# Kernel tuning notes

Measured on AMD Instinct MI355X. Metric: run time of the kernel, lower is better.

The kernel has to match this reference:

```python
import jax, jax.numpy as jnp
import numpy as np

B, S, D = 2, 1024, 4096
NQ, NKV, HD = 32, 8, 128
G = NQ // NKV
FFN = 10928  # ffn_size(4096, 4.0): int(4*4096)*2//3 = 10922 -> round up to mult of 8
ATTN_MULT = 0.08838834764831845
MAX_ATTN = 30.0
EPS = 1e-5
BASE = 10000.0


def setup_inputs() -> dict:
    key = jax.random.key(0)
    ks = jax.random.split(key, 13)
    def w(k, shape):
        return jax.random.normal(k, shape, jnp.float32) / np.float32(np.sqrt(shape[0]))
    return {
        "x": jax.random.normal(ks[0], (B, S, D), jnp.float32),
        "mask": jnp.tril(jnp.ones((1, 1, S, S), dtype=bool)),  # causal
        "scale_pre_attn": jax.random.uniform(ks[1], (D,), jnp.float32, 0.5, 1.5),
        "scale_post_attn": jax.random.uniform(ks[2], (D,), jnp.float32, 0.5, 1.5),
        "scale_pre_mlp": jax.random.uniform(ks[3], (D,), jnp.float32, 0.5, 1.5),
        "scale_post_mlp": jax.random.uniform(ks[4], (D,), jnp.float32, 0.5, 1.5),
        "wq": w(ks[5], (D, NQ * HD)),
        "wk": w(ks[6], (D, NKV * HD)),
        "wv": w(ks[7], (D, NKV * HD)),
        "wo": w(ks[8], (NQ * HD, D)),
        "w_gate": w(ks[9], (D, FFN)),
        "w_val": w(ks[10], (D, FFN)),
        "w_out": w(ks[11], (FFN, D)),
    }


def rms_norm(x, scale):
    ms = jnp.mean(jnp.square(x), axis=-1, keepdims=True)
    return x * jax.lax.rsqrt(ms + EPS) * scale


def rotate_half(x):
    x1, x2 = jnp.split(x, 2, axis=-1)
    return jnp.concatenate((-x2, x1), axis=-1)


def apply_rope(x):
    # x: [b, s, h, d]; offset=0 (no KV-cache step)
    s, d = x.shape[1], x.shape[3]
    inv_freq = 1.0 / (BASE ** (jnp.arange(0, d, 2, dtype=jnp.float32) / d))
    t = jnp.arange(s, dtype=jnp.float32)
    phase = t[:, None] * inv_freq[None, :]            # [s, d/2]
    phase = jnp.tile(phase, (1, 2))[None, :, None, :]  # [1, s, 1, d]
    return (x * jnp.cos(phase) + rotate_half(x) * jnp.sin(phase)).astype(x.dtype)


def reference(x, mask, scale_pre_attn, scale_post_attn, scale_pre_mlp, scale_post_mlp,
              wq, wk, wv, wo, w_gate, w_val, w_out):
    h = x
    # ---- attention sublayer (pre-norm) ----
    hn = rms_norm(h, scale_pre_attn)
    q = (hn @ wq).reshape(B, S, NQ, HD)
    k = (hn @ wk).reshape(B, S, NKV, HD)
    v = (hn @ wv).reshape(B, S, NKV, HD)
    q = apply_rope(q)
    k = apply_rope(k)
    qg = q.reshape(B, S, NKV, G, HD)  # GQA: group q heads per kv head
    logits = jnp.einsum("btkgd,bskd->bkgts", qg, k).astype(jnp.float32) * ATTN_MULT
    logits = MAX_ATTN * jnp.tanh(logits / MAX_ATTN)   # grok soft cap
    logits = jnp.where(mask[:, :, None], logits, -1e30)
    probs = jax.nn.softmax(logits, axis=-1).astype(x.dtype)
    attn = jnp.einsum("bkgts,bskd->btkgd", probs, v).reshape(B, S, NQ * HD)
    h_attn = attn @ wo
    h = h + rms_norm(h_attn, scale_post_attn)
    # ---- gated MLP sublayer (pre-norm) ----
    hn2 = rms_norm(h, scale_pre_mlp)
    h_dense = (jax.nn.gelu(hn2 @ w_gate) * (hn2 @ w_val)) @ w_out
    h = h + rms_norm(h_dense, scale_post_mlp)
    return h
```

## Files before the change

### kernel.cpp

```cpp
#include <hip/hip_runtime.h>
#include <stdint.h>

typedef unsigned short ushort_t;
typedef unsigned short us8 __attribute__((ext_vector_type(8)));
typedef __bf16 bf16x8 __attribute__((ext_vector_type(8)));
typedef float f32x4 __attribute__((ext_vector_type(4)));

#define D_MODEL 4096
#define SEQ 1024
#define BROWS 2048
#define QKV_N 6144
#define HD 128
#define FFN_GRID 11008
#define ATTN_MULT 0.08838834764831845f

__device__ __forceinline__ unsigned short f2bf(float f){
  union { float f; unsigned u; } c; c.f = f;
  unsigned u = c.u + 0x7fffu + ((c.u >> 16) & 1u);
  return (unsigned short)(u >> 16);
}
__device__ __forceinline__ float bf2f(unsigned short h){
  union { unsigned u; float f; } c; c.u = ((unsigned)h) << 16;
  return c.f;
}
__device__ __forceinline__ f32x4 zero4(){ f32x4 z; z[0]=0.f; z[1]=0.f; z[2]=0.f; z[3]=0.f; return z; }
__device__ __forceinline__ bf16x8 ldb8(const void* p){ return *(const bf16x8*)p; }
__device__ __forceinline__ f32x4 MFMA(bf16x8 a, bf16x8 b, f32x4 c){
  return __builtin_amdgcn_mfma_f32_16x16x32_bf16(a, b, c, 0, 0, 0);
}
__device__ __forceinline__ void g2lds16(void* lds, const void* g){
  __builtin_amdgcn_global_load_lds(
      (const __attribute__((address_space(1))) void*)(uintptr_t)(g),
      (__attribute__((address_space(3))) void*)(uint32_t)(uintptr_t)(lds),
      16, 0, 0);
}
#define BAR() __builtin_amdgcn_s_barrier()
#define VMCNT8() asm volatile("s_waitcnt vmcnt(8)" ::: "memory")
#define VMCNT0() asm volatile("s_waitcnt vmcnt(0)" ::: "memory")
#define SGB0() __builtin_amdgcn_sched_barrier(0)

__global__ __launch_bounds__(256) void rmsnorm_in(const float* __restrict__ x,
                                                  const float* __restrict__ sc,
                                                  ushort_t* __restrict__ out){
  int row = blockIdx.x, tid = threadIdx.x;
  const float4* xr = (const float4*)(x + (size_t)row*D_MODEL);
  float4 v[4]; float ss = 0.f;
#pragma unroll
  for (int i=0;i<4;i++){
    v[i] = xr[tid + i*256];
    ss += v[i].x*v[i].x + v[i].y*v[i].y + v[i].z*v[i].z + v[i].w*v[i].w;
  }
#pragma unroll
  for (int m=32;m;m>>=1) ss += __shfl_xor(ss, m);
  __shared__ float red[4];
  if ((tid&63)==0) red[tid>>6] = ss;
  __syncthreads();
  float inv = rsqrtf((red[0]+red[1]+red[2]+red[3])*(1.f/4096.f) + 1e-5f);
  const float4* scv = (const float4*)sc;
#pragma unroll
  for (int i=0;i<4;i++){
    float4 s4 = scv[tid + i*256];
    ushort4 o;
    o.x = f2bf(v[i].x*inv*s4.x); o.y = f2bf(v[i].y*inv*s4.y);
    o.z = f2bf(v[i].z*inv*s4.z); o.w = f2bf(v[i].w*inv*s4.w);
    ((ushort4*)out)[(size_t)row*1024 + tid + i*256] = o;
  }
}

__global__ __launch_bounds__(256) void rmsnorm_resid(const float* __restrict__ base,
                                                     const float* __restrict__ delta,
                                                     const float* __restrict__ delta2,
                                                     const float* __restrict__ sc1,
                                                     float* __restrict__ hout,
                                                     const float* __restrict__ sc2,
                                                     ushort_t* __restrict__ hn2){
  int row = blockIdx.x, tid = threadIdx.x;
  const float4* dr = (const float4*)(delta + (size_t)row*D_MODEL);
  const float4* d2 = delta2 ? (const float4*)(delta2 + (size_t)row*D_MODEL) : nullptr;
  const float4* br = (const float4*)(base  + (size_t)row*D_MODEL);
  float4 d[4]; float ss = 0.f;
#pragma unroll
  for (int i=0;i<4;i++){
    float4 a = dr[tid + i*256];
    if (d2){
      float4 b = d2[tid + i*256];
      a.x += b.x; a.y += b.y; a.z += b.z; a.w += b.w;
    }
    d[i] = a;
    ss += d[i].x*d[i].x + d[i].y*d[i].y + d[i].z*d[i].z + d[i].w*d[i].w;
  }
#pragma unroll
  for (int m=32;m;m>>=1) ss += __shfl_xor(ss, m);
  __shared__ float red[4];
  if ((tid&63)==0) red[tid>>6] = ss;
  __syncthreads();
  float inv1 = rsqrtf((red[0]+red[1]+red[2]+red[3])*(1.f/4096.f) + 1e-5f);
  const float4* s1v = (const float4*)sc1;
  float4* ho = (float4*)(hout + (size_t)row*D_MODEL);
  float4 h4[4]; float ss2 = 0.f;
#pragma unroll
  for (int i=0;i<4;i++){
    float4 b4 = br[tid + i*256];
    float4 s4 = s1v[tid + i*256];
    float4 h;
    h.x = b4.x + d[i].x*inv1*s4.x;
    h.y = b4.y + d[i].y*inv1*s4.y;
    h.z = b4.z + d[i].z*inv1*s4.z;
    h.w = b4.w + d[i].w*inv1*s4.w;
    h4[i] = h;
    ho[tid + i*256] = h;
    ss2 += h.x*h.x + h.y*h.y + h.z*h.z + h.w*h.w;
  }
  if (sc2){
#pragma unroll
    for (int m=32;m;m>>=1) ss2 += __shfl_xor(ss2, m);
    __syncthreads();
    if ((tid&63)==0) red[tid>>6] = ss2;
    __syncthreads();
    float inv2 = rsqrtf((red[0]+red[1]+red[2]+red[3])*(1.f/4096.f) + 1e-5f);
    const float4* s2v = (const float4*)sc2;
#pragma unroll
    for (int i=0;i<4;i++){
      float4 s4 = s2v[tid + i*256];
      ushort4 o;
      o.x = f2bf(h4[i].x*inv2*s4.x); o.y = f2bf(h4[i].y*inv2*s4.y);
      o.z = f2bf(h4[i].z*inv2*s4.z); o.w = f2bf(h4[i].w*inv2*s4.w);
      ((ushort4*)hn2)[(size_t)row*1024 + tid + i*256] = o;
    }
  }
}

__global__ __launch_bounds__(256) void convT(const float* __restrict__ W,
                                             ushort_t* __restrict__ WT,
                                             int K, int N, int Kp, int Np){
  __shared__ float tile[64][69];
  int tx = threadIdx.x & 15, ty = threadIdx.x >> 4;
  int n0 = blockIdx.x*64, k0 = blockIdx.y*64;
#pragma unroll
  for (int i=0;i<4;i++){
    int k = k0 + ty + i*16, n = n0 + tx*4;
    float4 v;
    if (k < K && n + 3 < N){
      v = *(const float4*)&W[(size_t)k*N + n];
    } else {
      v.x = (k<K && n+0<N) ? W[(size_t)k*N + n+0] : 0.f;
      v.y = (k<K && n+1<N) ? W[(size_t)k*N + n+1] : 0.f;
      v.z = (k<K && n+2<N) ? W[(size_t)k*N + n+2] : 0.f;
      v.w = (k<K && n+3<N) ? W[(size_t)k*N + n+3] : 0.f;
    }
    tile[ty+i*16][tx*4+0] = v.x;
    tile[ty+i*16][tx*4+1] = v.y;
    tile[ty+i*16][tx*4+2] = v.z;
    tile[ty+i*16][tx*4+3] = v.w;
  }
  __syncthreads();
  int kc = (threadIdx.x & 7)*8, nr = threadIdx.x >> 3;
#pragma unroll
  for (int j=0;j<2;j++){
    int n = n0 + nr + j*32;
    if (n < Np){
      us8 o;
#pragma unroll
      for (int i=0;i<8;i++) o[i] = f2bf(tile[kc+i][nr + j*32]);
      *(us8*)&WT[(size_t)n*Kp + k0 + kc] = o;
    }
  }
}

template<int MODE, int KS>
__global__ __launch_bounds__(512, 2) void gemmW(const ushort_t* __restrict__ A, int lda,
                                                const ushort_t* __restrict__ WT, int ldw,
                                                void* __restrict__ Cv, void* __restrict__ Cv2,
                                                int ldc, int Nvalid, int K){
  __shared__ __align__(16) char smem[131072];
  const int nwg = gridDim.x;
  const int lid = blockIdx.x;
  int t = (lid & 7) * (nwg >> 3) + (lid >> 3);
  void* Cout = Cv;
  if (KS == 2){
    const int per = nwg >> 1;
    if (t >= per){ t -= per; A += (size_t)K; WT += (size_t)K; Cout = Cv2; }
  }
  const int m0 = (t & 7) << 8;
  const int n0 = (t >> 3) << 8;
  const int tid = threadIdx.x;
  const int w = tid >> 6, lane = tid & 63;
  const int wm = w >> 1, wn = w & 1;
  const int lo = lane & 15, hi = lane >> 4;
  const int srow = lane >> 3, scol = lane & 7;
  const int sw = scol ^ srow;
  const int rsw = lo & 7;
  const int NT = K >> 6;

  const ushort_t* pA = A  + (size_t)(m0 + w*8 + srow) * lda + sw*8;
  const ushort_t* pB = WT + (size_t)(n0 + w*8 + srow) * ldw + sw*8;

  auto stage = [&](int tt, int c){
    const ushort_t* g = (c < 4 ? pA + (size_t)(c*64)*lda : pB + (size_t)((c-4)*64)*ldw) + (size_t)tt*64;
    g2lds16(smem + ((tt&1)<<16) + (c < 4 ? c*8192 : 32768 + (c-4)*8192) + (w<<10), g);
  };

  f32x4 acc[4][8];
#pragma unroll
  for (int i=0;i<4;i++)
#pragma unroll
    for (int j=0;j<8;j++) acc[i][j] = zero4();

#pragma unroll
  for (int c=0;c<8;c++) stage(0, c);
#pragma unroll
  for (int c=0;c<8;c++) stage(1, c);

  for (int i=0;i<NT;i++){
    if (i == NT-1) VMCNT0(); else VMCNT8();
    BAR();
    const char* sA = smem + ((i&1)<<16);
    const char* sB = sA + 32768;
    bf16x8 af[4][2], bfr[8][2];
#pragma unroll
    for (int rf=0;rf<4;rf++)
#pragma unroll
      for (int kc=0;kc<2;kc++)
        af[rf][kc] = ldb8(sA + (wm*64 + rf*16 + lo)*128 + (((kc*4+hi)^rsw)<<4));
#pragma unroll
    for (int cf=0;cf<8;cf++)
#pragma unroll
      for (int kc=0;kc<2;kc++)
        bfr[cf][kc] = ldb8(sB + (wn*128 + cf*16 + lo)*128 + (((kc*4+hi)^rsw)<<4));
#pragma unroll
    for (int rf=0;rf<4;rf++)
#pragma unroll
      for (int cf=0;cf<8;cf++)
#pragma unroll
        for (int kc=0;kc<2;kc++)
          acc[rf][cf] = MFMA(af[rf][kc], bfr[cf][kc], acc[rf][cf]);
    SGB0();
    BAR();
    if (i+2 < NT){
#pragma unroll
      for (int c=0;c<8;c++) stage(i+2, c);
    }
  }
#pragma unroll
  for (int rf=0;rf<4;rf++){
#pragma unroll
    for (int cf=0;cf<8;cf++){
#pragma unroll
      for (int r=0;r<4;r++){
        int m = m0 + wm*64 + rf*16 + hi*4 + r;
        int n = n0 + wn*128 + cf*16 + lo;
        if (n < Nvalid){
          float v = acc[rf][cf][r];
          size_t idx = (size_t)m*ldc + n;
          if (MODE == 1) ((float*)Cout)[idx] = v;
          else           ((ushort_t*)Cout)[idx] = f2bf(v);
        }
      }
    }
  }
}

__global__ __launch_bounds__(512, 2) void gemm_gv(const ushort_t* __restrict__ A, int lda,
                                                  const ushort_t* __restrict__ B1,
                                                  const ushort_t* __restrict__ B2, int ldw,
                                                  ushort_t* __restrict__ Cv, int ldc,
                                                  int Nvalid, int K){
  __shared__ __align__(16) char smem[131072];
  const int nwg = gridDim.x;
  const int lid = blockIdx.x;
  const int t  = (lid & 7) * (nwg >> 3) + (lid >> 3);
  const int m0 = (t & 7) << 8;
  const int n0 = (t >> 3) << 7;
  const int tid = threadIdx.x;
  const int w = tid >> 6, lane = tid & 63;
  const int wm = w >> 1, wn = w & 1;
  const int lo = lane & 15, hi = lane >> 4;
  const int srow = lane >> 3, scol = lane & 7;
  const int sw = scol ^ srow;
  const int rsw = lo & 7;
  const int NT = K >> 6;

  const ushort_t* pA  = A  + (size_t)(m0 + w*8 + srow) * lda + sw*8;
  const ushort_t* pB1 = B1 + (size_t)(n0 + w*8 + srow) * ldw + sw*8;
  const ushort_t* pB2 = B2 + (size_t)(n0 + w*8 + srow) * ldw + sw*8;

  auto stage = [&](int tt, int c){
    const ushort_t* g;
    int lofs;
    if (c < 4){ g = pA  + (size_t)(c*64)*lda;     lofs = c*8192; }
    else if (c < 6){ g = pB1 + (size_t)((c-4)*64)*ldw; lofs = 32768 + (c-4)*8192; }
    else { g = pB2 + (size_t)((c-6)*64)*ldw; lofs = 49152 + (c-6)*8192; }
    g2lds16(smem + ((tt&1)<<16) + lofs + (w<<10), g + (size_t)tt*64);
  };

  f32x4 ag[4][4], av[4][4];
#pragma unroll
  for (int i=0;i<4;i++)
#pragma unroll
    for (int j=0;j<4;j++){ ag[i][j] = zero4(); av[i][j] = zero4(); }

#pragma unroll
  for (int c=0;c<8;c++) stage(0, c);
#pragma unroll
  for (int c=0;c<8;c++) stage(1, c);

  for (int i=0;i<NT;i++){
    if (i == NT-1) VMCNT0(); else VMCNT8();
    BAR();
    const char* sA  = smem + ((i&1)<<16);
    const char* sB1 = sA + 32768;
    const char* sB2 = sA + 49152;
    bf16x8 af[4][2], b1f[4][2], b2f[4][2];
#pragma unroll
    for (int rf=0;rf<4;rf++)
#pragma unroll
      for (int kc=0;kc<2;kc++)
        af[rf][kc] = ldb8(sA + (wm*64 + rf*16 + lo)*128 + (((kc*4+hi)^rsw)<<4));
#pragma unroll
    for (int cf=0;cf<4;cf++)
#pragma unroll
      for (int kc=0;kc<2;kc++){
        b1f[cf][kc] = ldb8(sB1 + (wn*64 + cf*16 + lo)*128 + (((kc*4+hi)^rsw)<<4));
        b2f[cf][kc] = ldb8(sB2 + (wn*64 + cf*16 + lo)*128 + (((kc*4+hi)^rsw)<<4));
      }
#pragma unroll
    for (int rf=0;rf<4;rf++)
#pragma unroll
      for (int cf=0;cf<4;cf++)
#pragma unroll
        for (int kc=0;kc<2;kc++){
          ag[rf][cf] = MFMA(af[rf][kc], b1f[cf][kc], ag[rf][cf]);
          av[rf][cf] = MFMA(af[rf][kc], b2f[cf][kc], av[rf][cf]);
        }
    SGB0();
    BAR();
    if (i+2 < NT){
#pragma unroll
      for (int c=0;c<8;c++) stage(i+2, c);
    }
  }
#pragma unroll
  for (int rf=0;rf<4;rf++){
#pragma unroll
    for (int cf=0;cf<4;cf++){
#pragma unroll
      for (int r=0;r<4;r++){
        int m = m0 + wm*64 + rf*16 + hi*4 + r;
        int n = n0 + wn*64 + cf*16 + lo;
        if (n < Nvalid){
          float g = ag[rf][cf][r];
          float v = av[rf][cf][r];
          float ga = 0.5f*g*(1.f + tanhf(0.7978845608028654f*(g + 0.044715f*g*g*g)));
          Cv[(size_t)m*ldc + n] = f2bf(ga * v);
        }
      }
    }
  }
}

__global__ void rope_tab_kernel(float* __restrict__ tab){
  int s = blockIdx.x, i = threadIdx.x;
  float invf = __expf(-(float)i * (9.210340371976184f/64.f));
  float ph = (float)s * invf;
  float sn, cs;
  sincosf(ph, &sn, &cs);
  tab[s*128 + i] = cs;
  tab[s*128 + 64 + i] = sn;
}

__global__ __launch_bounds__(256) void rope_apply(ushort_t* __restrict__ qkv,
                                                  const float* __restrict__ tab){
  int idx = blockIdx.x*256 + threadIdx.x;
  int pr = idx & 63;
  int h  = (idx >> 6) % 40;
  int row = idx / 2560;
  int t = row & (SEQ-1);
  ushort_t* p = qkv + (size_t)row*QKV_N + h*HD + pr;
  float c = tab[t*128 + pr], s = tab[t*128 + 64 + pr];
  float x1 = bf2f(p[0]), x2 = bf2f(p[64]);
  p[0]  = f2bf(x1*c - x2*s);
  p[64] = f2bf(x2*c + x1*s);
}

__global__ __launch_bounds__(256) void transpose_v(const ushort_t* __restrict__ qkv,
                                                   ushort_t* __restrict__ VT){
  __shared__ ushort_t tile[32][33];
  int d0 = blockIdx.x*32, m0 = blockIdx.y*32;
  int tx = threadIdx.x & 31, ty = threadIdx.x >> 5;
#pragma unroll
  for (int i=0;i<4;i++)
    tile[ty + i*8][tx] = qkv[(size_t)(m0 + ty + i*8)*QKV_N + 5120 + d0 + tx];
  __syncthreads();
#pragma unroll
  for (int i=0;i<4;i++)
    VT[(size_t)(d0 + ty + i*8)*BROWS + m0 + tx] = tile[tx][ty + i*8];
}

__global__ __launch_bounds__(256) void attn_kernel(const ushort_t* __restrict__ qkv,
                                                   const ushort_t* __restrict__ VT,
                                                   ushort_t* __restrict__ outp){
  const int blk = blockIdx.x;
  const int bh = blk & 63;
  const int tgrp = 15 - (blk >> 6);
  const int b = bh >> 5, qh = bh & 31, kv = qh >> 2;
  const int w = threadIdx.x >> 6, lane = threadIdx.x & 63;
  const int lo = lane & 15, hi = lane >> 4;
  const int t0 = tgrp*64 + w*16;
  __shared__ ushort_t P[4][16][72];
  ushort_t (*Pw)[72] = P[w];

  const ushort_t* Qb = qkv + (size_t)(b*SEQ + t0 + lo)*QKV_N + qh*HD + hi*8;
  bf16x8 qf[4];
#pragma unroll
  for (int c=0;c<4;c++) qf[c] = ldb8(Qb + c*32);

  f32x4 of[8];
#pragma unroll
  for (int i=0;i<8;i++) of[i] = zero4();
  float ls[4] = {0.f,0.f,0.f,0.f};

  const ushort_t* Kb = qkv + (size_t)(b*SEQ + lo)*QKV_N + D_MODEL + kv*HD + hi*8;
  const ushort_t* Vb = VT + (size_t)(kv*HD + lo)*BROWS + b*SEQ + hi*8;

  const int nst = tgrp + 1;
  for (int st=0; st<nst; st++){
    const int s0 = st*64;
    f32x4 sacc[4];
#pragma unroll
    for (int nf=0;nf<4;nf++) sacc[nf] = zero4();
#pragma unroll
    for (int c=0;c<4;c++){
#pragma unroll
      for (int nf=0;nf<4;nf++){
        bf16x8 kf = ldb8(Kb + (size_t)(s0 + nf*16)*QKV_N + c*32);
        sacc[nf] = MFMA(qf[c], kf, sacc[nf]);
      }
    }
#pragma unroll
    for (int nf=0;nf<4;nf++){
#pragma unroll
      for (int r=0;r<4;r++){
        int tq = t0 + hi*4 + r;
        int s = s0 + nf*16 + lo;
        float xx = sacc[nf][r] * ATTN_MULT;
        float z = fminf(fmaxf(xx*(2.f/30.f), -80.f), 80.f);
        float e = __expf(z);
        float th = (e - 1.f)/(e + 1.f);
        float p = (s <= tq) ? __expf(30.f*th - 30.f) : 0.f;
        ls[r] += p;
        Pw[hi*4+r][nf*16+lo] = f2bf(p);
      }
    }
    __builtin_amdgcn_sched_barrier(0);
    __builtin_amdgcn_s_waitcnt(0xc07f);
    __builtin_amdgcn_sched_barrier(0);
#pragma unroll
    for (int c2=0;c2<2;c2++){
      bf16x8 pf = ldb8(&Pw[lo][c2*32 + hi*8]);
#pragma unroll
      for (int nf2=0;nf2<8;nf2++){
        bf16x8 vf = ldb8(Vb + (size_t)(nf2*16)*BROWS + s0 + c2*32);
        of[nf2] = MFMA(pf, vf, of[nf2]);
      }
    }
    __builtin_amdgcn_sched_barrier(0);
  }
#pragma unroll
  for (int m=1;m<16;m<<=1){
#pragma unroll
    for (int r=0;r<4;r++) ls[r] += __shfl_xor(ls[r], m);
  }
  float inv[4];
#pragma unroll
  for (int r=0;r<4;r++) inv[r] = 1.f/ls[r];
  ushort_t* Ob = outp + (size_t)(b*SEQ + t0 + hi*4)*D_MODEL + qh*HD + lo;
#pragma unroll
  for (int nf2=0;nf2<8;nf2++)
#pragma unroll
    for (int r=0;r<4;r++)
      Ob[(size_t)r*D_MODEL + nf2*16] = f2bf(of[nf2][r]*inv[r]);
}

extern "C" void kernel_launch(void* const* d_in, const int* in_sizes, int n_in,
                              void* d_out, int out_size, void* d_ws, size_t ws_size,
                              hipStream_t stream){
  const float* x        = (const float*)d_in[0];
  const float* sc_pre_a = (const float*)d_in[2];
  const float* sc_post_a= (const float*)d_in[3];
  const float* sc_pre_m = (const float*)d_in[4];
  const float* sc_post_m= (const float*)d_in[5];
  const float* wq  = (const float*)d_in[6];
  const float* wk  = (const float*)d_in[7];
  const float* wv  = (const float*)d_in[8];
  const float* wo  = (const float*)d_in[9];
  const float* wg  = (const float*)d_in[10];
  const float* wva = (const float*)d_in[11];
  const float* wou = (const float*)d_in[12];

  char* ws = (char*)d_ws;
  size_t off = 0;
  auto alloc = [&](size_t bytes)->void*{
    void* p = ws + off; off += (bytes + 255) & ~(size_t)255; return p;
  };
  ushort_t* WT   = (ushort_t*)alloc((size_t)FFN_GRID*D_MODEL*2);
  ushort_t* hn   = (ushort_t*)alloc((size_t)BROWS*D_MODEL*2);
  ushort_t* qkv  = (ushort_t*)alloc((size_t)BROWS*QKV_N*2);
  ushort_t* VT   = (ushort_t*)alloc((size_t)SEQ*BROWS*2);
  ushort_t* attn = (ushort_t*)alloc((size_t)BROWS*D_MODEL*2);
  float*    tmp32= (float*)alloc((size_t)BROWS*D_MODEL*4);
  ushort_t* hn2  = (ushort_t*)alloc((size_t)BROWS*D_MODEL*2);
  ushort_t* act  = (ushort_t*)alloc((size_t)BROWS*FFN_GRID*2);
  float*    rtab = (float*)alloc((size_t)SEQ*128*4);
  float* h = (float*)d_out;
  ushort_t* WT2  = (ushort_t*)hn;
  float* part_o  = (float*)act;
  float* part_u  = (float*)hn;

  rmsnorm_in<<<BROWS, 256, 0, stream>>>(x, sc_pre_a, hn);
  convT<<<dim3(64, 64), 256, 0, stream>>>(wq, WT,                     4096, 4096, 4096, 4096);
  convT<<<dim3(16, 64), 256, 0, stream>>>(wk, WT + (size_t)4096*4096, 4096, 1024, 4096, 1024);
  convT<<<dim3(16, 64), 256, 0, stream>>>(wv, WT + (size_t)5120*4096, 4096, 1024, 4096, 1024);
  gemmW<0,1><<<192, 512, 0, stream>>>(hn, 4096, WT, 4096, qkv, nullptr, QKV_N, QKV_N, 4096);
  rope_tab_kernel<<<SEQ, 64, 0, stream>>>(rtab);
  rope_apply<<<(BROWS*40*64)/256, 256, 0, stream>>>(qkv, rtab);
  transpose_v<<<dim3(32,64), 256, 0, stream>>>(qkv, VT);
  attn_kernel<<<1024, 256, 0, stream>>>(qkv, VT, attn);
  convT<<<dim3(64, 64), 256, 0, stream>>>(wo, WT, 4096, 4096, 4096, 4096);
  gemmW<1,2><<<256, 512, 0, stream>>>(attn, 4096, WT, 4096, tmp32, part_o, 4096, 4096, 2048);
  rmsnorm_resid<<<BROWS, 256, 0, stream>>>(x, tmp32, part_o, sc_post_a, h, sc_pre_m, hn2);
  convT<<<dim3(172, 64), 256, 0, stream>>>(wg,  WT,  4096, 10928, 4096, FFN_GRID);
  convT<<<dim3(172, 64), 256, 0, stream>>>(wva, WT2, 4096, 10928, 4096, FFN_GRID);
  gemm_gv<<<688, 512, 0, stream>>>(hn2, 4096, WT, WT2, 4096, act, FFN_GRID, FFN_GRID, 4096);
  convT<<<dim3(64, 172), 256, 0, stream>>>(wou, WT, 10928, 4096, FFN_GRID, 4096);
  gemmW<1,2><<<256, 512, 0, stream>>>(act, FFN_GRID, WT, FFN_GRID, tmp32, part_u, 4096, 4096, 5504);
  rmsnorm_resid<<<BROWS, 256, 0, stream>>>(h, tmp32, part_u, sc_post_m, h, nullptr, nullptr);
}
```

Measured before the change: 1.162 ms.

## Issue next-stage loads before MFMAs and use 192-wide N tiles for QKV

The GEMM main loops now wait for the LDS fragment reads, place a barrier, and issue the global-to-LDS prefetch for stage i+2 before the MFMA block. Previously the prefetch was issued after the MFMAs, so the next loads now overlap with compute. The gemmW kernel is templated on the N tile width, and the QKV projection uses 192-wide tiles with 256 workgroups instead of 192 workgroups, so every CU gets work. This adds an extra barrier per iteration and changes the vmcnt accounting for the 6-fragment variant, which could stall if it is miscounted.

After: 1.105 ms, median of 3. 1.05x faster.

```diff
diff --git a/kernel.cpp b/kernel.cpp
--- a/kernel.cpp
+++ b/kernel.cpp
@@ -36,8 +36,9 @@
 }
 #define BAR() __builtin_amdgcn_s_barrier()
 #define VMCNT8() asm volatile("s_waitcnt vmcnt(8)" ::: "memory")
+#define VMCNT7() asm volatile("s_waitcnt vmcnt(7)" ::: "memory")
 #define VMCNT0() asm volatile("s_waitcnt vmcnt(0)" ::: "memory")
-#define SGB0() __builtin_amdgcn_sched_barrier(0)
+#define LGKM0() asm volatile("s_waitcnt lgkmcnt(0)" ::: "memory")
 
 __global__ __launch_bounds__(256) void rmsnorm_in(const float* __restrict__ x,
                                                   const float* __restrict__ sc,
@@ -167,12 +168,15 @@
   }
 }
 
-template<int MODE, int KS>
+template<int MODE, int KS, int CF>
 __global__ __launch_bounds__(512, 2) void gemmW(const ushort_t* __restrict__ A, int lda,
                                                 const ushort_t* __restrict__ WT, int ldw,
                                                 void* __restrict__ Cv, void* __restrict__ Cv2,
                                                 int ldc, int Nvalid, int K){
-  __shared__ __align__(16) char smem[131072];
+  constexpr int BN   = CF*32;
+  constexpr int NCH  = 4 + CF/2;
+  constexpr int SLOT = 32768 + (CF/2)*8192;
+  __shared__ __align__(16) char smem[2*SLOT];
   const int nwg = gridDim.x;
   const int lid = blockIdx.x;
   int t = (lid & 7) * (nwg >> 3) + (lid >> 3);
@@ -182,7 +186,7 @@
     if (t >= per){ t -= per; A += (size_t)K; WT += (size_t)K; Cout = Cv2; }
   }
   const int m0 = (t & 7) << 8;
-  const int n0 = (t >> 3) << 8;
+  const int n0 = (t >> 3) * BN;
   const int tid = threadIdx.x;
   const int w = tid >> 6, lane = tid & 63;
   const int wm = w >> 1, wn = w & 1;
@@ -197,58 +201,59 @@
 
   auto stage = [&](int tt, int c){
     const ushort_t* g = (c < 4 ? pA + (size_t)(c*64)*lda : pB + (size_t)((c-4)*64)*ldw) + (size_t)tt*64;
-    g2lds16(smem + ((tt&1)<<16) + (c < 4 ? c*8192 : 32768 + (c-4)*8192) + (w<<10), g);
+    g2lds16(smem + (tt&1)*SLOT + (c < 4 ? c*8192 : 32768 + (c-4)*8192) + (w<<10), g);
   };
 
-  f32x4 acc[4][8];
+  f32x4 acc[4][CF];
 #pragma unroll
   for (int i=0;i<4;i++)
 #pragma unroll
-    for (int j=0;j<8;j++) acc[i][j] = zero4();
-
-#pragma unroll
-  for (int c=0;c<8;c++) stage(0, c);
-#pragma unroll
-  for (int c=0;c<8;c++) stage(1, c);
+    for (int j=0;j<CF;j++) acc[i][j] = zero4();
+
+#pragma unroll
+  for (int c=0;c<NCH;c++) stage(0, c);
+#pragma unroll
+  for (int c=0;c<NCH;c++) stage(1, c);
 
   for (int i=0;i<NT;i++){
-    if (i == NT-1) VMCNT0(); else VMCNT8();
+    if (i == NT-1) { VMCNT0(); }
+    else if (CF == 8) { VMCNT8(); } else { VMCNT7(); }
     BAR();
-    const char* sA = smem + ((i&1)<<16);
+    const char* sA = smem + (i&1)*SLOT;
     const char* sB = sA + 32768;
-    bf16x8 af[4][2], bfr[8][2];
+    bf16x8 af[4][2], bfr[CF][2];
 #pragma unroll
     for (int rf=0;rf<4;rf++)
 #pragma unroll
       for (int kc=0;kc<2;kc++)
         af[rf][kc] = ldb8(sA + (wm*64 + rf*16 + lo)*128 + (((kc*4+hi)^rsw)<<4));
 #pragma unroll
-    for (int cf=0;cf<8;cf++)
+    for (int cf=0;cf<CF;cf++)
 #pragma unroll
       for (int kc=0;kc<2;kc++)
-        bfr[cf][kc] = ldb8(sB + (wn*128 + cf*16 + lo)*128 + (((kc*4+hi)^rsw)<<4));
+        bfr[cf][kc] = ldb8(sB + (wn*(CF*16) + cf*16 + lo)*128 + (((kc*4+hi)^rsw)<<4));
+    LGKM0();
+    BAR();
+    if (i+2 < NT){
+#pragma unroll
+      for (int c=0;c<NCH;c++) stage(i+2, c);
+    }
 #pragma unroll
     for (int rf=0;rf<4;rf++)
 #pragma unroll
-      for (int cf=0;cf<8;cf++)
+      for (int cf=0;cf<CF;cf++)
 #pragma unroll
         for (int kc=0;kc<2;kc++)
           acc[rf][cf] = MFMA(af[rf][kc], bfr[cf][kc], acc[rf][cf]);
-    SGB0();
-    BAR();
-    if (i+2 < NT){
-#pragma unroll
-      for (int c=0;c<8;c++) stage(i+2, c);
-    }
   }
 #pragma unroll
   for (int rf=0;rf<4;rf++){
 #pragma unroll
-    for (int cf=0;cf<8;cf++){
+    for (int cf=0;cf<CF;cf++){
 #pragma unroll
       for (int r=0;r<4;r++){
         int m = m0 + wm*64 + rf*16 + hi*4 + r;
-        int n = n0 + wn*128 + cf*16 + lo;
+        int n = n0 + wn*(CF*16) + cf*16 + lo;
         if (n < Nvalid){
           float v = acc[rf][cf][r];
           size_t idx = (size_t)m*ldc + n;
@@ -323,6 +328,12 @@
         b1f[cf][kc] = ldb8(sB1 + (wn*64 + cf*16 + lo)*128 + (((kc*4+hi)^rsw)<<4));
         b2f[cf][kc] = ldb8(sB2 + (wn*64 + cf*16 + lo)*128 + (((kc*4+hi)^rsw)<<4));
       }
+    LGKM0();
+    BAR();
+    if (i+2 < NT){
+#pragma unroll
+      for (int c=0;c<8;c++) stage(i+2, c);
+    }
 #pragma unroll
     for (int rf=0;rf<4;rf++)
 #pragma unroll
@@ -332,12 +343,6 @@
           ag[rf][cf] = MFMA(af[rf][kc], b1f[cf][kc], ag[rf][cf]);
           av[rf][cf] = MFMA(af[rf][kc], b2f[cf][kc], av[rf][cf]);
         }
-    SGB0();
-    BAR();
-    if (i+2 < NT){
-#pragma unroll
-      for (int c=0;c<8;c++) stage(i+2, c);
-    }
   }
 #pragma unroll
   for (int rf=0;rf<4;rf++){
@@ -520,18 +525,18 @@
   convT<<<dim3(64, 64), 256, 0, stream>>>(wq, WT,                     4096, 4096, 4096, 4096);
   convT<<<dim3(16, 64), 256, 0, stream>>>(wk, WT + (size_t)4096*4096, 4096, 1024, 4096, 1024);
   convT<<<dim3(16, 64), 256, 0, stream>>>(wv, WT + (size_t)5120*4096, 4096, 1024, 4096, 1024);
-  gemmW<0,1><<<192, 512, 0, stream>>>(hn, 4096, WT, 4096, qkv, nullptr, QKV_N, QKV_N, 4096);
+  gemmW<0,1,6><<<256, 512, 0, stream>>>(hn, 4096, WT, 4096, qkv, nullptr, QKV_N, QKV_N, 4096);
   rope_tab_kernel<<<SEQ, 64, 0, stream>>>(rtab);
   rope_apply<<<(BROWS*40*64)/256, 256, 0, stream>>>(qkv, rtab);
   transpose_v<<<dim3(32,64), 256, 0, stream>>>(qkv, VT);
   attn_kernel<<<1024, 256, 0, stream>>>(qkv, VT, attn);
   convT<<<dim3(64, 64), 256, 0, stream>>>(wo, WT, 4096, 4096, 4096, 4096);
-  gemmW<1,2><<<256, 512, 0, stream>>>(attn, 4096, WT, 4096, tmp32, part_o, 4096, 4096, 2048);
+  gemmW<1,2,8><<<256, 512, 0, stream>>>(attn, 4096, WT, 4096, tmp32, part_o, 4096, 4096, 2048);
   rmsnorm_resid<<<BROWS, 256, 0, stream>>>(x, tmp32, part_o, sc_post_a, h, sc_pre_m, hn2);
   convT<<<dim3(172, 64), 256, 0, stream>>>(wg,  WT,  4096, 10928, 4096, FFN_GRID);
   convT<<<dim3(172, 64), 256, 0, stream>>>(wva, WT2, 4096, 10928, 4096, FFN_GRID);
   gemm_gv<<<688, 512, 0, stream>>>(hn2, 4096, WT, WT2, 4096, act, FFN_GRID, FFN_GRID, 4096);
   convT<<<dim3(64, 172), 256, 0, stream>>>(wou, WT, 10928, 4096, FFN_GRID, 4096);
-  gemmW<1,2><<<256, 512, 0, stream>>>(act, FFN_GRID, WT, FFN_GRID, tmp32, part_u, 4096, 4096, 5504);
+  gemmW<1,2,8><<<256, 512, 0, stream>>>(act, FFN_GRID, WT, FFN_GRID, tmp32, part_u, 4096, 4096, 5504);
   rmsnorm_resid<<<BROWS, 256, 0, stream>>>(h, tmp32, part_u, sc_post_m, h, nullptr, nullptr);
 }
```

## Shrink GEMM tiles to 256x128xK32, raise occupancy, and unfuse gate/value GEMM

Applied to the files above, without the earlier changes.

The main GEMM kernel now uses 256x128 output tiles with a K-step of 32 and 48KB of LDS in place of 128KB. Launch bounds go from 2 to 4 blocks, and grids double to keep the same coverage. The LDS fragment loads now complete before the barrier, and the next stage is prefetched before the MFMAs are issued. The fused gate/value GEMM with its GELU epilogue is replaced by two separate GEMMs plus an elementwise gelu_mul kernel. This adds extra memory traffic for the value activations and halves per-tile data reuse, in exchange for higher occupancy and latency hiding.

New measurement: 1.245 ms. 1.07x slower.

```diff
diff --git a/kernel.cpp b/kernel.cpp
--- a/kernel.cpp
+++ b/kernel.cpp
@@ -35,9 +35,9 @@
       16, 0, 0);
 }
 #define BAR() __builtin_amdgcn_s_barrier()
-#define VMCNT8() asm volatile("s_waitcnt vmcnt(8)" ::: "memory")
+#define VMCNT3() asm volatile("s_waitcnt vmcnt(3)" ::: "memory")
 #define VMCNT0() asm volatile("s_waitcnt vmcnt(0)" ::: "memory")
-#define SGB0() __builtin_amdgcn_sched_barrier(0)
+#define LGKM0() asm volatile("s_waitcnt lgkmcnt(0)" ::: "memory")
 
 __global__ __launch_bounds__(256) void rmsnorm_in(const float* __restrict__ x,
                                                   const float* __restrict__ sc,
@@ -168,11 +168,11 @@
 }
 
 template<int MODE, int KS>
-__global__ __launch_bounds__(512, 2) void gemmW(const ushort_t* __restrict__ A, int lda,
+__global__ __launch_bounds__(512, 4) void gemmW(const ushort_t* __restrict__ A, int lda,
                                                 const ushort_t* __restrict__ WT, int ldw,
                                                 void* __restrict__ Cv, void* __restrict__ Cv2,
                                                 int ldc, int Nvalid, int K){
-  __shared__ __align__(16) char smem[131072];
+  __shared__ __align__(16) char smem[49152];
   const int nwg = gridDim.x;
   const int lid = blockIdx.x;
   int t = (lid & 7) * (nwg >> 3) + (lid >> 3);
@@ -182,73 +182,67 @@
     if (t >= per){ t -= per; A += (size_t)K; WT += (size_t)K; Cout = Cv2; }
   }
   const int m0 = (t & 7) << 8;
-  const int n0 = (t >> 3) << 8;
+  const int n0 = (t >> 3) << 7;
   const int tid = threadIdx.x;
   const int w = tid >> 6, lane = tid & 63;
   const int wm = w >> 1, wn = w & 1;
   const int lo = lane & 15, hi = lane >> 4;
-  const int srow = lane >> 3, scol = lane & 7;
-  const int sw = scol ^ srow;
-  const int rsw = lo & 7;
-  const int NT = K >> 6;
-
-  const ushort_t* pA = A  + (size_t)(m0 + w*8 + srow) * lda + sw*8;
-  const ushort_t* pB = WT + (size_t)(n0 + w*8 + srow) * ldw + sw*8;
+  const int rsw2 = (lo >> 1) & 3;
+  const int strow = tid >> 2;
+  const int sseg  = (tid & 3) ^ ((tid >> 3) & 3);
+  const int NT = K >> 5;
 
   auto stage = [&](int tt, int c){
-    const ushort_t* g = (c < 4 ? pA + (size_t)(c*64)*lda : pB + (size_t)((c-4)*64)*ldw) + (size_t)tt*64;
-    g2lds16(smem + ((tt&1)<<16) + (c < 4 ? c*8192 : 32768 + (c-4)*8192) + (w<<10), g);
+    const ushort_t* g;
+    int lofs;
+    if (c < 2){ g = A  + (size_t)(m0 + c*128 + strow)*lda; lofs = c*8192; }
+    else      { g = WT + (size_t)(n0 + strow)*ldw;         lofs = 16384; }
+    g2lds16(smem + (tt&1)*24576 + lofs + (w<<10),
+            g + (size_t)tt*32 + sseg*8);
   };
 
-  f32x4 acc[4][8];
+  f32x4 acc[4][4];
 #pragma unroll
   for (int i=0;i<4;i++)
 #pragma unroll
-    for (int j=0;j<8;j++) acc[i][j] = zero4();
-
-#pragma unroll
-  for (int c=0;c<8;c++) stage(0, c);
-#pragma unroll
-  for (int c=0;c<8;c++) stage(1, c);
+    for (int j=0;j<4;j++) acc[i][j] = zero4();
+
+#pragma unroll
+  for (int c=0;c<3;c++) stage(0, c);
+#pragma unroll
+  for (int c=0;c<3;c++) stage(1, c);
 
   for (int i=0;i<NT;i++){
-    if (i == NT-1) VMCNT0(); else VMCNT8();
+    if (i == NT-1) VMCNT0(); else VMCNT3();
     BAR();
-    const char* sA = smem + ((i&1)<<16);
-    const char* sB = sA + 32768;
-    bf16x8 af[4][2], bfr[8][2];
+    const char* sA = smem + (i&1)*24576;
+    const char* sB = sA + 16384;
+    bf16x8 af[4], bfr[4];
 #pragma unroll
     for (int rf=0;rf<4;rf++)
-#pragma unroll
-      for (int kc=0;kc<2;kc++)
-        af[rf][kc] = ldb8(sA + (wm*64 + rf*16 + lo)*128 + (((kc*4+hi)^rsw)<<4));
-#pragma unroll
-    for (int cf=0;cf<8;cf++)
-#pragma unroll
-      for (int kc=0;kc<2;kc++)
-        bfr[cf][kc] = ldb8(sB + (wn*128 + cf*16 + lo)*128 + (((kc*4+hi)^rsw)<<4));
-#pragma unroll
-    for (int rf=0;rf<4;rf++)
-#pragma unroll
-      for (int cf=0;cf<8;cf++)
-#pragma unroll
-        for (int kc=0;kc<2;kc++)
-          acc[rf][cf] = MFMA(af[rf][kc], bfr[cf][kc], acc[rf][cf]);
-    SGB0();
+      af[rf] = ldb8(sA + (wm*64 + rf*16 + lo)*64 + ((hi^rsw2)<<4));
+#pragma unroll
+    for (int cf=0;cf<4;cf++)
+      bfr[cf] = ldb8(sB + (wn*64 + cf*16 + lo)*64 + ((hi^rsw2)<<4));
+    LGKM0();
     BAR();
     if (i+2 < NT){
-#pragma unroll
-      for (int c=0;c<8;c++) stage(i+2, c);
-    }
+      stage(i+2, 0); stage(i+2, 1); stage(i+2, 2);
+    }
+#pragma unroll
+    for (int rf=0;rf<4;rf++)
+#pragma unroll
+      for (int cf=0;cf<4;cf++)
+        acc[rf][cf] = MFMA(af[rf], bfr[cf], acc[rf][cf]);
   }
 #pragma unroll
   for (int rf=0;rf<4;rf++){
 #pragma unroll
-    for (int cf=0;cf<8;cf++){
+    for (int cf=0;cf<4;cf++){
 #pragma unroll
       for (int r=0;r<4;r++){
         int m = m0 + wm*64 + rf*16 + hi*4 + r;
-        int n = n0 + wn*128 + cf*16 + lo;
+        int n = n0 + wn*64 + cf*16 + lo;
         if (n < Nvalid){
           float v = acc[rf][cf][r];
           size_t idx = (size_t)m*ldc + n;
@@ -260,101 +254,23 @@
   }
 }
 
-__global__ __launch_bounds__(512, 2) void gemm_gv(const ushort_t* __restrict__ A, int lda,
-                                                  const ushort_t* __restrict__ B1,
-                                                  const ushort_t* __restrict__ B2, int ldw,
-                                                  ushort_t* __restrict__ Cv, int ldc,
-                                                  int Nvalid, int K){
-  __shared__ __align__(16) char smem[131072];
-  const int nwg = gridDim.x;
-  const int lid = blockIdx.x;
-  const int t  = (lid & 7) * (nwg >> 3) + (lid >> 3);
-  const int m0 = (t & 7) << 8;
-  const int n0 = (t >> 3) << 7;
-  const int tid = threadIdx.x;
-  const int w = tid >> 6, lane = tid & 63;
-  const int wm = w >> 1, wn = w & 1;
-  const int lo = lane & 15, hi = lane >> 4;
-  const int srow = lane >> 3, scol = lane & 7;
-  const int sw = scol ^ srow;
-  const int rsw = lo & 7;
-  const int NT = K >> 6;
-
-  const ushort_t* pA  = A  + (size_t)(m0 + w*8 + srow) * lda + sw*8;
-  const ushort_t* pB1 = B1 + (size_t)(n0 + w*8 + srow) * ldw + sw*8;
-  const ushort_t* pB2 = B2 + (size_t)(n0 + w*8 + srow) * ldw + sw*8;
-
-  auto stage = [&](int tt, int c){
-    const ushort_t* g;
-    int lofs;
-    if (c < 4){ g = pA  + (size_t)(c*64)*lda;     lofs = c*8192; }
-    else if (c < 6){ g = pB1 + (size_t)((c-4)*64)*ldw; lofs = 32768 + (c-4)*8192; }
-    else { g = pB2 + (size_t)((c-6)*64)*ldw; lofs = 49152 + (c-6)*8192; }
-    g2lds16(smem + ((tt&1)<<16) + lofs + (w<<10), g + (size_t)tt*64);
-  };
-
-  f32x4 ag[4][4], av[4][4];
-#pragma unroll
-  for (int i=0;i<4;i++)
-#pragma unroll
-    for (int j=0;j<4;j++){ ag[i][j] = zero4(); av[i][j] = zero4(); }
-
-#pragma unroll
-  for (int c=0;c<8;c++) stage(0, c);
-#pragma unroll
-  for (int c=0;c<8;c++) stage(1, c);
-
-  for (int i=0;i<NT;i++){
-    if (i == NT-1) VMCNT0(); else VMCNT8();
-    BAR();
-    const char* sA  = smem + ((i&1)<<16);
-    const char* sB1 = sA + 32768;
-    const char* sB2 = sA + 49152;
-    bf16x8 af[4][2], b1f[4][2], b2f[4][2];
-#pragma unroll
-    for (int rf=0;rf<4;rf++)
-#pragma unroll
-      for (int kc=0;kc<2;kc++)
-        af[rf][kc] = ldb8(sA + (wm*64 + rf*16 + lo)*128 + (((kc*4+hi)^rsw)<<4));
-#pragma unroll
-    for (int cf=0;cf<4;cf++)
-#pragma unroll
-      for (int kc=0;kc<2;kc++){
-        b1f[cf][kc] = ldb8(sB1 + (wn*64 + cf*16 + lo)*128 + (((kc*4+hi)^rsw)<<4));
-        b2f[cf][kc] = ldb8(sB2 + (wn*64 + cf*16 + lo)*128 + (((kc*4+hi)^rsw)<<4));
-      }
-#pragma unroll
-    for (int rf=0;rf<4;rf++)
-#pragma unroll
-      for (int cf=0;cf<4;cf++)
-#pragma unroll
-        for (int kc=0;kc<2;kc++){
-          ag[rf][cf] = MFMA(af[rf][kc], b1f[cf][kc], ag[rf][cf]);
-          av[rf][cf] = MFMA(af[rf][kc], b2f[cf][kc], av[rf][cf]);
-        }
-    SGB0();
-    BAR();
-    if (i+2 < NT){
-#pragma unroll
-      for (int c=0;c<8;c++) stage(i+2, c);
-    }
-  }
-#pragma unroll
-  for (int rf=0;rf<4;rf++){
-#pragma unroll
-    for (int cf=0;cf<4;cf++){
-#pragma unroll
-      for (int r=0;r<4;r++){
-        int m = m0 + wm*64 + rf*16 + hi*4 + r;
-        int n = n0 + wn*64 + cf*16 + lo;
-        if (n < Nvalid){
-          float g = ag[rf][cf][r];
-          float v = av[rf][cf][r];
-          float ga = 0.5f*g*(1.f + tanhf(0.7978845608028654f*(g + 0.044715f*g*g*g)));
-          Cv[(size_t)m*ldc + n] = f2bf(ga * v);
-        }
-      }
-    }
+__global__ __launch_bounds__(256) void gelu_mul(const ushort_t* __restrict__ G,
+                                               const ushort_t* __restrict__ V,
+                                               ushort_t* __restrict__ O, long n8){
+  long i = (long)blockIdx.x*256 + threadIdx.x;
+  const long stride = (long)gridDim.x*256;
+  for (; i < n8; i += stride){
+    us8 g8 = ((const us8*)G)[i];
+    us8 v8 = ((const us8*)V)[i];
+    us8 o;
+#pragma unroll
+    for (int j=0;j<8;j++){
+      float g = bf2f(g8[j]);
+      float v = bf2f(v8[j]);
+      float ga = 0.5f*g*(1.f + tanhf(0.7978845608028654f*(g + 0.044715f*g*g*g)));
+      o[j] = f2bf(ga * v);
+    }
+    ((us8*)O)[i] = o;
   }
 }
 
@@ -510,6 +426,7 @@
   float*    tmp32= (float*)alloc((size_t)BROWS*D_MODEL*4);
   ushort_t* hn2  = (ushort_t*)alloc((size_t)BROWS*D_MODEL*2);
   ushort_t* act  = (ushort_t*)alloc((size_t)BROWS*FFN_GRID*2);
+  ushort_t* actV = (ushort_t*)alloc((size_t)BROWS*FFN_GRID*2);
   float*    rtab = (float*)alloc((size_t)SEQ*128*4);
   float* h = (float*)d_out;
   ushort_t* WT2  = (ushort_t*)hn;
@@ -520,18 +437,20 @@
   convT<<<dim3(64, 64), 256, 0, stream>>>(wq, WT,                     4096, 4096, 4096, 4096);
   convT<<<dim3(16, 64), 256, 0, stream>>>(wk, WT + (size_t)4096*4096, 4096, 1024, 4096, 1024);
   convT<<<dim3(16, 64), 256, 0, stream>>>(wv, WT + (size_t)5120*4096, 4096, 1024, 4096, 1024);
-  gemmW<0,1><<<192, 512, 0, stream>>>(hn, 4096, WT, 4096, qkv, nullptr, QKV_N, QKV_N, 4096);
+  gemmW<0,1><<<384, 512, 0, stream>>>(hn, 4096, WT, 4096, qkv, nullptr, QKV_N, QKV_N, 4096);
   rope_tab_kernel<<<SEQ, 64, 0, stream>>>(rtab);
   rope_apply<<<(BROWS*40*64)/256, 256, 0, stream>>>(qkv, rtab);
   transpose_v<<<dim3(32,64), 256, 0, stream>>>(qkv, VT);
   attn_kernel<<<1024, 256, 0, stream>>>(qkv, VT, attn);
   convT<<<dim3(64, 64), 256, 0, stream>>>(wo, WT, 4096, 4096, 4096, 4096);
-  gemmW<1,2><<<256, 512, 0, stream>>>(attn, 4096, WT, 4096, tmp32, part_o, 4096, 4096, 2048);
+  gemmW<1,2><<<512, 512, 0, stream>>>(attn, 4096, WT, 4096, tmp32, part_o, 4096, 4096, 2048);
   rmsnorm_resid<<<BROWS, 256, 0, stream>>>(x, tmp32, part_o, sc_post_a, h, sc_pre_m, hn2);
   convT<<<dim3(172, 64), 256, 0, stream>>>(wg,  WT,  4096, 10928, 4096, FFN_GRID);
   convT<<<dim3(172, 64), 256, 0, stream>>>(wva, WT2, 4096, 10928, 4096, FFN_GRID);
-  gemm_gv<<<688, 512, 0, stream>>>(hn2, 4096, WT, WT2, 4096, act, FFN_GRID, FFN_GRID, 4096);
+  gemmW<0,1><<<688, 512, 0, stream>>>(hn2, 4096, WT,  4096, act,  nullptr, FFN_GRID, FFN_GRID, 4096);
+  gemmW<0,1><<<688, 512, 0, stream>>>(hn2, 4096, WT2, 4096, actV, nullptr, FFN_GRID, FFN_GRID, 4096);
+  gelu_mul<<<2048, 256, 0, stream>>>(act, actV, act, (long)BROWS*FFN_GRID/8);
   convT<<<dim3(64, 172), 256, 0, stream>>>(wou, WT, 10928, 4096, FFN_GRID, 4096);
-  gemmW<1,2><<<256, 512, 0, stream>>>(act, FFN_GRID, WT, FFN_GRID, tmp32, part_u, 4096, 4096, 5504);
+  gemmW<1,2><<<512, 512, 0, stream>>>(act, FFN_GRID, WT, FFN_GRID, tmp32, part_u, 4096, 4096, 5504);
   rmsnorm_resid<<<BROWS, 256, 0, stream>>>(h, tmp32, part_u, sc_post_m, h, nullptr, nullptr);
 }
```
